# Performance work log

Hardware: AMD Instinct MI355X
Metric: run time of the kernel (lower is better)

## Reference

```python
import jax, jax.numpy as jnp
import numpy as np
from jax import lax

KSIZE = 3
STRIDE = 1
RATE = 2
FUSE_K = 3
SCALE = 10.0
DN = ('NCHW', 'OIHW', 'NCHW')


def _same_pad_amount(size, k, s):
    out = (size + s - 1) // s
    pad = max(0, (out - 1) * s + k - size)
    return pad // 2, pad - pad // 2


def extract_patches(x, k, s):
    # torch.nn.Unfold with 'same' padding; returns [B, L, C, k, k], L row-major
    B, C, H, W = x.shape
    pt, pb = _same_pad_amount(H, k, s)
    pl, pr = _same_pad_amount(W, k, s)
    xp = jnp.pad(x, ((0, 0), (0, 0), (pt, pb), (pl, pr)))
    Ho = (H + s - 1) // s
    Wo = (W + s - 1) // s
    rows = (jnp.arange(Ho) * s)[:, None] + jnp.arange(k)[None, :]  # [Ho,k]
    cols = (jnp.arange(Wo) * s)[:, None] + jnp.arange(k)[None, :]  # [Wo,k]
    p = xp[:, :, rows, :][:, :, :, :, cols]  # [B,C,Ho,k,Wo,k]
    return p.transpose(0, 2, 4, 1, 3, 5).reshape(B, Ho * Wo, C, k, k)


def setup_inputs() -> dict:
    key = jax.random.key(0)
    kf, kb = jax.random.split(key)
    f = jax.random.normal(kf, (2, 128, 128, 128), dtype=jnp.float32)
    b = jax.random.normal(kb, (2, 128, 128, 128), dtype=jnp.float32)
    mask = jnp.zeros((1, 1, 128, 128), dtype=jnp.float32)  # all patches available
    return {"f": f, "b": b, "mask": mask}


def reference(f, b, mask):
    B, C, Hr, Wr = f.shape
    kernel = 2 * RATE
    # raw background patches for final aggregation: [B, Lb, C, 4, 4]
    raw_w = extract_patches(b, kernel, RATE * STRIDE)
    # nearest downsample by rate (src_idx = i*rate)
    f_ds = f[:, :, ::RATE, ::RATE]
    b_ds = b[:, :, ::RATE, ::RATE]
    Hf, Wf = f_ds.shape[2], f_ds.shape[3]
    Hb, Wb = b_ds.shape[2], b_ds.shape[3]
    L = Hb * Wb
    # matching patches: [B, L, C, 3, 3]
    w = extract_patches(b_ds, KSIZE, STRIDE)
    # mask patches (shared across batch, torch uses m[0])
    m_ds = mask[:, :, ::RATE, ::RATE]
    m = extract_patches(m_ds, KSIZE, STRIDE)[0]  # [L,1,3,3]
    mm = (jnp.mean(m, axis=(1, 2, 3)) == 0.0).astype(f.dtype).reshape(1, L, 1, 1)
    # L2-normalize patch filters (escape_NaN added elementwise before sum, as in torch)
    wn = w / jnp.sqrt(jnp.sum(w * w + 1e-4, axis=(2, 3, 4), keepdims=True))

    def score_one(xi, wi):
        # xi [C,Hf,Wf], wi [L,C,3,3] -> [L,Hf,Wf]
        return lax.conv_general_dilated(xi[None], wi, (1, 1), [(1, 1), (1, 1)],
                                        dimension_numbers=DN)[0]

    y = jax.vmap(score_one)(f_ds, wn)  # [B, L, Hf, Wf]

    # diagonal fuse: identity 3x3 conv on the [L, Hf*Wf] score matrix, twice with transpose
    fw = jnp.eye(FUSE_K, dtype=f.dtype).reshape(1, 1, FUSE_K, FUSE_K)

    def fuse_conv(t):
        return lax.conv_general_dilated(t, fw, (1, 1), [(1, 1), (1, 1)],
                                        dimension_numbers=DN)

    y = y.reshape(B, 1, Hb * Wb, Hf * Wf)
    y = fuse_conv(y).reshape(B, Hb, Wb, Hf, Wf)
    y = y.transpose(0, 2, 1, 4, 3).reshape(B, 1, L, Hf * Wf)
    y = fuse_conv(y).reshape(B, Wb, Hb, Wf, Hf)
    y = y.transpose(0, 2, 1, 4, 3).reshape(B, L, Hf, Wf)

    y = y * mm
    y = jax.nn.softmax(y * SCALE, axis=1) * mm

    def deconv_one(a, wc):
        # conv_transpose2d(a, wc, stride=rate, padding=1); wc [L,C,4,4]
        wt = jnp.flip(wc, (-2, -1)).transpose(1, 0, 2, 3)  # [C,L,4,4]
        pad = kernel - 1 - 1
        return lax.conv_general_dilated(a[None], wt, (1, 1), [(pad, pad), (pad, pad)],
                                        lhs_dilation=(RATE, RATE),
                                        dimension_numbers=DN)[0]

    out = jax.vmap(deconv_one)(y, raw_w) / 4.0  # [B, C, Hr, Wr]
    return out
```

## Files before the change

kernel.cpp:

```cpp
#include <hip/hip_runtime.h>
#include <cstdint>

typedef _Float16 f16x8 __attribute__((ext_vector_type(8)));
typedef float f32x4 __attribute__((ext_vector_type(4)));

typedef __attribute__((address_space(1))) void gvoid;
typedef __attribute__((address_space(3))) void lvoid;

__device__ __forceinline__ void gload16(const void* g, void* l) {
    __builtin_amdgcn_global_load_lds((gvoid*)g, (lvoid*)l, 16, 0, 0);
}

__global__ __launch_bounds__(256) void downsample_kernel(const float* __restrict__ f,
                                                         const float* __restrict__ b,
                                                         float* __restrict__ fds,
                                                         float* __restrict__ bds) {
    int idx = blockIdx.x * 256 + threadIdx.x;
    const float* src = blockIdx.y ? b : f;
    float* dst = blockIdx.y ? bds : fds;
    int bb = idx >> 19;
    int r = idx & 524287;
    int c = r >> 12, a = (r >> 6) & 63, v = r & 63;
    dst[idx] = src[(size_t)bb * 2097152 + (size_t)c * 16384 + (2 * a) * 128 + 2 * v];
}

__global__ __launch_bounds__(256) void build_mm_kernel(const float* __restrict__ mask,
                                                       float* __restrict__ mm) {
    int l = blockIdx.x * 256 + threadIdx.x;
    if (l >= 4096) return;
    int i = l >> 6, j = l & 63;
    float s = 0.f;
    #pragma unroll
    for (int dy = 0; dy < 3; ++dy)
        #pragma unroll
        for (int dx = 0; dx < 3; ++dx) {
            int a = i + dy - 1, b = j + dx - 1;
            if ((unsigned)a < 64u && (unsigned)b < 64u)
                s += mask[(2 * a) * 128 + 2 * b];
        }
    mm[l] = (s == 0.0f) ? 1.0f : 0.0f;
}

__global__ __launch_bounds__(256) void build_fpatch_kernel(const float* __restrict__ fds,
                                                           _Float16* __restrict__ Fp) {
    int bb = blockIdx.x >> 12;
    int p = blockIdx.x & 4095;
    const float* fb = fds + (size_t)bb * 524288;
    _Float16* Fpb = Fp + (size_t)bb * 4718592;
    int u = p >> 6, v = p & 63;
    for (int k = threadIdx.x; k < 1152; k += 256) {
        int c = k / 9;
        int s = k - 9 * c;
        int dy = s / 3, dx = s - 3 * dy;
        int a = u + dy - 1, bcol = v + dx - 1;
        float val = 0.f;
        if ((unsigned)a < 64u && (unsigned)bcol < 64u)
            val = fb[c * 4096 + a * 64 + bcol];
        Fpb[(size_t)p * 1152 + k] = (_Float16)val;
    }
}

__global__ __launch_bounds__(256) void build_wn_kernel(const float* __restrict__ bds,
                                                       _Float16* __restrict__ Wn) {
    __shared__ float wsh[1152];
    __shared__ float red[4];
    int bb = blockIdx.x >> 12;
    int l = blockIdx.x & 4095;
    const float* bp = bds + (size_t)bb * 524288;
    _Float16* Wnb = Wn + (size_t)bb * 4718592;
    int i = l >> 6, j = l & 63;
    float sq = 0.f;
    for (int k = threadIdx.x; k < 1152; k += 256) {
        int c = k / 9;
        int s = k - 9 * c;
        int dy = s / 3, dx = s - 3 * dy;
        int a = i + dy - 1, bcol = j + dx - 1;
        float val = 0.f;
        if ((unsigned)a < 64u && (unsigned)bcol < 64u)
            val = bp[c * 4096 + a * 64 + bcol];
        wsh[k] = val;
        sq += val * val;
    }
    #pragma unroll
    for (int off = 32; off > 0; off >>= 1) sq += __shfl_xor(sq, off);
    if ((threadIdx.x & 63) == 0) red[threadIdx.x >> 6] = sq;
    __syncthreads();
    float total = red[0] + red[1] + red[2] + red[3] + 0.1152f;
    float rinv = 1.0f / sqrtf(total);
    for (int k = threadIdx.x; k < 1152; k += 256)
        Wnb[(size_t)l * 1152 + k] = (_Float16)(wsh[k] * rinv);
}

__global__ __launch_bounds__(256) void build_vt_kernel(const float* __restrict__ b,
                                                       _Float16* __restrict__ Vt) {
    int bb = blockIdx.x >> 11;
    int n = blockIdx.x & 2047;
    const float* bp = b + (size_t)bb * 2097152;
    _Float16* Vtb = Vt + (size_t)bb * 8388608;
    int c = n >> 4, r = n & 15, rh = r >> 2, rw = r & 3;
    const float* bc = bp + (size_t)c * 16384;
    for (int l = threadIdx.x; l < 4096; l += 256) {
        int lh = l >> 6, lw = l & 63;
        int row = 2 * lh + rh - 1, col = 2 * lw + rw - 1;
        float val = 0.f;
        if ((unsigned)row < 128u && (unsigned)col < 128u)
            val = bc[row * 128 + col];
        Vtb[(size_t)n * 4096 + l] = (_Float16)val;
    }
}

__global__ __launch_bounds__(256) void gemm1_kernel(const _Float16* __restrict__ Fp,
                                                    const _Float16* __restrict__ Wn,
                                                    _Float16* __restrict__ S0) {
    __shared__ __align__(16) _Float16 As[128 * 32];
    __shared__ __align__(16) _Float16 Bs[128 * 32];
    const int z = blockIdx.z;
    const _Float16* A = Fp + (size_t)z * 4718592;
    const _Float16* Bt = Wn + (size_t)z * 4718592;
    _Float16* C = S0 + (size_t)z * 16777216;
    const int tid = threadIdx.x;
    const int lane = tid & 63;
    const int wave = tid >> 6;
    const int quad = lane >> 4;
    const int l16 = lane & 15;
    const int bm = blockIdx.y * 128;
    const int bn = blockIdx.x * 128;
    const int waveM = (wave >> 1) * 64;
    const int waveN = (wave & 1) * 64;
    const int K = 1152;

    f32x4 acc[4][4] = {};

    const int rowS = tid >> 2;
    const int colS = (tid & 3) * 8;

    for (int k0 = 0; k0 < K; k0 += 32) {
        #pragma unroll
        for (int i = 0; i < 2; ++i) {
            const _Float16* g = A + (size_t)(bm + i * 64 + rowS) * K + k0 + colS;
            gload16(g, &As[i * 2048 + tid * 8]);
        }
        #pragma unroll
        for (int i = 0; i < 2; ++i) {
            const _Float16* g = Bt + (size_t)(bn + i * 64 + rowS) * K + k0 + colS;
            gload16(g, &Bs[i * 2048 + tid * 8]);
        }
        __syncthreads();
        f16x8 a_frag[4], b_frag[4];
        #pragma unroll
        for (int mi = 0; mi < 4; ++mi)
            a_frag[mi] = *(const f16x8*)&As[(waveM + mi * 16 + l16) * 32 + quad * 8];
        #pragma unroll
        for (int ni = 0; ni < 4; ++ni)
            b_frag[ni] = *(const f16x8*)&Bs[(waveN + ni * 16 + l16) * 32 + quad * 8];
        #pragma unroll
        for (int mi = 0; mi < 4; ++mi)
            #pragma unroll
            for (int ni = 0; ni < 4; ++ni)
                acc[mi][ni] = __builtin_amdgcn_mfma_f32_16x16x32_f16(
                    a_frag[mi], b_frag[ni], acc[mi][ni], 0, 0, 0);
        __syncthreads();
    }

    #pragma unroll
    for (int mi = 0; mi < 4; ++mi)
        #pragma unroll
        for (int ni = 0; ni < 4; ++ni)
            #pragma unroll
            for (int r = 0; r < 4; ++r) {
                int row = bm + waveM + mi * 16 + quad * 4 + r;
                int col = bn + waveN + ni * 16 + l16;
                C[(size_t)row * 4096 + col] = (_Float16)acc[mi][ni][r];
            }
}

__global__ __launch_bounds__(256) void gemm2_kernel(const _Float16* __restrict__ Vt,
                                                    const _Float16* __restrict__ att0,
                                                    const _Float16* __restrict__ att1,
                                                    _Float16* __restrict__ OTh) {
    __shared__ __align__(16) _Float16 As[128 * 64];
    __shared__ __align__(16) _Float16 Bs[128 * 64];
    const int z = blockIdx.z;
    const _Float16* A = Vt + (size_t)z * 8388608;
    const _Float16* Bt = z ? att1 : att0;
    _Float16* C = OTh + (size_t)z * 8388608;
    const int tid = threadIdx.x;
    const int lane = tid & 63;
    const int wave = tid >> 6;
    const int quad = lane >> 4;
    const int l16 = lane & 15;
    const int bm = blockIdx.y * 128;
    const int bn = blockIdx.x * 128;
    const int waveM = (wave >> 1) * 64;
    const int waveN = (wave & 1) * 64;
    const int K = 4096;

    f32x4 acc[4][4] = {};

    const int rowS = tid >> 3;
    const int cbs = ((tid & 7) ^ (rowS & 7)) * 8;

    for (int k0 = 0; k0 < K; k0 += 64) {
        #pragma unroll
        for (int i = 0; i < 4; ++i) {
            const _Float16* g = A + (size_t)(bm + i * 32 + rowS) * K + k0 + cbs;
            gload16(g, &As[i * 2048 + tid * 8]);
        }
        #pragma unroll
        for (int i = 0; i < 4; ++i) {
            const _Float16* g = Bt + (size_t)(bn + i * 32 + rowS) * K + k0 + cbs;
            gload16(g, &Bs[i * 2048 + tid * 8]);
        }
        __syncthreads();
        #pragma unroll
        for (int h = 0; h < 2; ++h) {
            f16x8 a_frag[4], b_frag[4];
            #pragma unroll
            for (int mi = 0; mi < 4; ++mi) {
                int r = waveM + mi * 16 + l16;
                int q = h * 4 + quad;
                a_frag[mi] = *(const f16x8*)&As[r * 64 + ((q ^ (r & 7)) * 8)];
            }
            #pragma unroll
            for (int ni = 0; ni < 4; ++ni) {
                int r = waveN + ni * 16 + l16;
                int q = h * 4 + quad;
                b_frag[ni] = *(const f16x8*)&Bs[r * 64 + ((q ^ (r & 7)) * 8)];
            }
            #pragma unroll
            for (int mi = 0; mi < 4; ++mi)
                #pragma unroll
                for (int ni = 0; ni < 4; ++ni)
                    acc[mi][ni] = __builtin_amdgcn_mfma_f32_16x16x32_f16(
                        a_frag[mi], b_frag[ni], acc[mi][ni], 0, 0, 0);
        }
        __syncthreads();
    }

    #pragma unroll
    for (int mi = 0; mi < 4; ++mi)
        #pragma unroll
        for (int ni = 0; ni < 4; ++ni)
            #pragma unroll
            for (int r = 0; r < 4; ++r) {
                int row = bm + waveM + mi * 16 + quad * 4 + r;
                int col = bn + waveN + ni * 16 + l16;
                C[(size_t)row * 4096 + col] = (_Float16)acc[mi][ni][r];
            }
}

__global__ __launch_bounds__(256) void fuse_softmax_kernel(const _Float16* __restrict__ S0,
                                                           const float* __restrict__ mm,
                                                           _Float16* __restrict__ att0,
                                                           _Float16* __restrict__ att1) {
    __shared__ float red[4];
    const int tid = threadIdx.x;
    const int lane = tid & 63;
    const int wave = tid >> 6;
    int g = blockIdx.x;
    int p_global = ((g & 7) << 10) | (g >> 3);
    const int bb = p_global >> 12;
    const int p = p_global & 4095;
    const _Float16* S = S0 + (size_t)bb * 16777216;
    _Float16* att = bb ? att1 : att0;
    const int pbase = ((p & 63) << 6) | (p >> 6);

    float acc[16];
    #pragma unroll
    for (int k = 0; k < 16; ++k) acc[k] = 0.f;

    #pragma unroll
    for (int t2 = -1; t2 <= 1; ++t2) {
        int b2 = pbase + t2;
        if ((unsigned)b2 >= 4096u) continue;
        int pp = ((b2 & 63) << 6) | (b2 >> 6);
        #pragma unroll
        for (int t1 = -1; t1 <= 1; ++t1) {
            int rr = pp + t1;
            if ((unsigned)rr >= 4096u) continue;
            const _Float16* row = S + (size_t)rr * 4096;
            #pragma unroll
            for (int k = 0; k < 16; ++k) {
                int l = k * 256 + tid;
                int i = (k * 256 + wave * 64) >> 6;
                int it2 = i + t2;
                if (it2 >= 0 && it2 < 64) {
                    int c = l + t2 * 64 + t1;
                    if ((unsigned)c < 4096u)
                        acc[k] += (float)row[c];
                } else if (it2 == 64) {
                    if (lane <= 62) {
                        int c = lane + 1 + t1;
                        if ((unsigned)c < 4096u) acc[k] += (float)row[c];
                    }
                } else {
                    if (lane >= 1) {
                        int c = 4031 + lane + t1;
                        if ((unsigned)c < 4096u) acc[k] += (float)row[c];
                    }
                }
            }
        }
    }

    float mv[16];
    float lmax = -1e30f;
    #pragma unroll
    for (int k = 0; k < 16; ++k) {
        int l = k * 256 + tid;
        mv[k] = mm[l];
        float lg = acc[k] * mv[k] * 10.0f;
        acc[k] = lg;
        lmax = fmaxf(lmax, lg);
    }
    #pragma unroll
    for (int off = 32; off > 0; off >>= 1) lmax = fmaxf(lmax, __shfl_xor(lmax, off));
    if (lane == 0) red[wave] = lmax;
    __syncthreads();
    lmax = fmaxf(fmaxf(red[0], red[1]), fmaxf(red[2], red[3]));
    __syncthreads();

    float lsum = 0.f;
    #pragma unroll
    for (int k = 0; k < 16; ++k) {
        float e = __expf(acc[k] - lmax);
        acc[k] = e;
        lsum += e;
    }
    #pragma unroll
    for (int off = 32; off > 0; off >>= 1) lsum += __shfl_xor(lsum, off);
    if (lane == 0) red[wave] = lsum;
    __syncthreads();
    float inv = 1.0f / (red[0] + red[1] + red[2] + red[3]);
    #pragma unroll
    for (int k = 0; k < 16; ++k) {
        int l = k * 256 + tid;
        att[(size_t)p * 4096 + l] = (_Float16)(acc[k] * inv * mv[k]);
    }
}

__global__ __launch_bounds__(256) void assemble_kernel(const _Float16* __restrict__ OTh,
                                                       float* __restrict__ out) {
    int idx = blockIdx.x * 256 + threadIdx.x;
    int bb = idx >> 21;
    int w = idx & 2097151;
    const _Float16* OTb = OTh + (size_t)bb * 8388608;
    int x = w & 127, y = (w >> 7) & 127, c = w >> 14;
    int r0 = (y + 1) & 1, s0 = (x + 1) & 1;
    float acc = 0.f;
    #pragma unroll
    for (int a = 0; a < 2; ++a) {
        int rh = r0 + 2 * a;
        int ph = (y + 1 - rh) >> 1;
        if ((unsigned)ph < 64u) {
            #pragma unroll
            for (int bq = 0; bq < 2; ++bq) {
                int rw = s0 + 2 * bq;
                int pw = (x + 1 - rw) >> 1;
                if ((unsigned)pw < 64u)
                    acc += (float)OTb[(size_t)(c * 16 + rh * 4 + rw) * 4096 + ph * 64 + pw];
            }
        }
    }
    out[idx] = 0.25f * acc;
}

extern "C" void kernel_launch(void* const* d_in, const int* in_sizes, int n_in,
                              void* d_out, int out_size, void* d_ws, size_t ws_size,
                              hipStream_t stream) {
    const float* f = (const float*)d_in[0];
    const float* b = (const float*)d_in[1];
    const float* mask = (const float*)d_in[2];
    float* out = (float*)d_out;
    char* ws = (char*)d_ws;

    float* mm = (float*)ws;
    _Float16* Fp = (_Float16*)(ws + 16384);
    _Float16* Wn = (_Float16*)(ws + 16384 + 18874368);
    _Float16* att0 = (_Float16*)(ws + 16384);
    _Float16* S0 = (_Float16*)(ws + 37765120);
    _Float16* Vt = (_Float16*)(ws + 37765120);
    _Float16* OTh = (_Float16*)(ws + 37765120 + 33554432);
    float* fds = (float*)(ws + 104873984);
    float* bds = (float*)(ws + 104873984 + 4194304);
    _Float16* att1 = (_Float16*)(ws + 104873984);

    downsample_kernel<<<dim3(4096, 2), 256, 0, stream>>>(f, b, fds, bds);
    build_mm_kernel<<<16, 256, 0, stream>>>(mask, mm);
    build_fpatch_kernel<<<8192, 256, 0, stream>>>(fds, Fp);
    build_wn_kernel<<<8192, 256, 0, stream>>>(bds, Wn);

    gemm1_kernel<<<dim3(32, 32, 2), 256, 0, stream>>>(Fp, Wn, S0);
    fuse_softmax_kernel<<<8192, 256, 0, stream>>>(S0, mm, att0, att1);

    build_vt_kernel<<<4096, 256, 0, stream>>>(b, Vt);
    gemm2_kernel<<<dim3(32, 16, 2), 256, 0, stream>>>(Vt, att0, att1, OTh);
    assemble_kernel<<<16384, 256, 0, stream>>>(OTh, out);
}
```

Measured before the change: 464.9 us.

## Rewrite gemm2 with 256x256 tiles, 8 waves and double-buffered LDS pipeline

The second GEMM (Vt x attention) moves from 128x128 tiles with 4 waves and a single LDS buffer to 256x256 tiles with 8 waves. It adds double-buffered async global-to-LDS loads interleaved with MFMA phases, using explicit vmcnt waits, raw barriers, s_setprio around MFMA bursts and a new LDS swizzle. The aim is to hide global load latency and raise arithmetic intensity per tile. The risks are higher register pressure from the 32 accumulators and fewer blocks (256 total) relative to the CU count.

```diff
diff --git a/kernel.cpp b/kernel.cpp
--- a/kernel.cpp
+++ b/kernel.cpp
@@ -10,6 +10,13 @@
 __device__ __forceinline__ void gload16(const void* g, void* l) {
     __builtin_amdgcn_global_load_lds((gvoid*)g, (lvoid*)l, 16, 0, 0);
 }
+
+__device__ __forceinline__ void bar() {
+    asm volatile("" ::: "memory");
+    __builtin_amdgcn_s_barrier();
+    asm volatile("" ::: "memory");
+}
+#define WAITV(N) asm volatile("s_waitcnt vmcnt(" #N ")" ::: "memory")
 
 __global__ __launch_bounds__(256) void downsample_kernel(const float* __restrict__ f,
                                                          const float* __restrict__ b,
@@ -174,12 +181,12 @@
             }
 }
 
-__global__ __launch_bounds__(256) void gemm2_kernel(const _Float16* __restrict__ Vt,
-                                                    const _Float16* __restrict__ att0,
-                                                    const _Float16* __restrict__ att1,
-                                                    _Float16* __restrict__ OTh) {
-    __shared__ __align__(16) _Float16 As[128 * 64];
-    __shared__ __align__(16) _Float16 Bs[128 * 64];
+__global__ __launch_bounds__(512, 2) void gemm2_kernel(const _Float16* __restrict__ Vt,
+                                                       const _Float16* __restrict__ att0,
+                                                       const _Float16* __restrict__ att1,
+                                                       _Float16* __restrict__ OTh) {
+    __shared__ __align__(16) _Float16 As[2][2][8192];
+    __shared__ __align__(16) _Float16 Bs[2][2][8192];
     const int z = blockIdx.z;
     const _Float16* A = Vt + (size_t)z * 8388608;
     const _Float16* Bt = z ? att1 : att0;
@@ -189,62 +196,109 @@
     const int wave = tid >> 6;
     const int quad = lane >> 4;
     const int l16 = lane & 15;
-    const int bm = blockIdx.y * 128;
-    const int bn = blockIdx.x * 128;
-    const int waveM = (wave >> 1) * 64;
-    const int waveN = (wave & 1) * 64;
-    const int K = 4096;
-
-    f32x4 acc[4][4] = {};
-
-    const int rowS = tid >> 3;
-    const int cbs = ((tid & 7) ^ (rowS & 7)) * 8;
-
-    for (int k0 = 0; k0 < K; k0 += 64) {
-        #pragma unroll
-        for (int i = 0; i < 4; ++i) {
-            const _Float16* g = A + (size_t)(bm + i * 32 + rowS) * K + k0 + cbs;
-            gload16(g, &As[i * 2048 + tid * 8]);
-        }
-        #pragma unroll
-        for (int i = 0; i < 4; ++i) {
-            const _Float16* g = Bt + (size_t)(bn + i * 32 + rowS) * K + k0 + cbs;
-            gload16(g, &Bs[i * 2048 + tid * 8]);
-        }
-        __syncthreads();
-        #pragma unroll
-        for (int h = 0; h < 2; ++h) {
-            f16x8 a_frag[4], b_frag[4];
-            #pragma unroll
-            for (int mi = 0; mi < 4; ++mi) {
-                int r = waveM + mi * 16 + l16;
-                int q = h * 4 + quad;
-                a_frag[mi] = *(const f16x8*)&As[r * 64 + ((q ^ (r & 7)) * 8)];
-            }
-            #pragma unroll
-            for (int ni = 0; ni < 4; ++ni) {
-                int r = waveN + ni * 16 + l16;
-                int q = h * 4 + quad;
-                b_frag[ni] = *(const f16x8*)&Bs[r * 64 + ((q ^ (r & 7)) * 8)];
-            }
-            #pragma unroll
-            for (int mi = 0; mi < 4; ++mi)
-                #pragma unroll
-                for (int ni = 0; ni < 4; ++ni)
-                    acc[mi][ni] = __builtin_amdgcn_mfma_f32_16x16x32_f16(
-                        a_frag[mi], b_frag[ni], acc[mi][ni], 0, 0, 0);
-        }
-        __syncthreads();
-    }
-
-    #pragma unroll
-    for (int mi = 0; mi < 4; ++mi)
+    const int wm = wave >> 2;
+    const int wn = wave & 3;
+    const int bm = blockIdx.y * 256;
+    const int bn = blockIdx.x * 256;
+
+    f32x4 acc[8][4] = {};
+    f16x8 afr[4], bfr[4];
+
+    const int s0 = tid, s1 = 512 + tid;
+    const int sr0 = s0 >> 2, sr1 = s1 >> 2;
+    const int r0 = sr0 ^ ((sr0 >> 2) & 1);
+    const int r1 = sr1 ^ ((sr1 >> 2) & 1);
+    const int q0 = (s0 & 3) ^ (r0 & 3);
+    const int q1 = (s1 & 3) ^ (r1 & 3);
+    const int offA0 = (bm + r0) * 4096 + q0 * 8;
+    const int offA1 = (bm + r1) * 4096 + q1 * 8;
+    const int offB0 = (bn + r0) * 4096 + q0 * 8;
+    const int offB1 = (bn + r1) * 4096 + q1 * 8;
+
+#define STAGE_A(buf, kt, kh) do {                                          \
+        gload16(A + offA0 + (kt) * 64 + (kh) * 32, &As[buf][kh][tid * 8]); \
+        gload16(A + offA1 + (kt) * 64 + (kh) * 32, &As[buf][kh][4096 + tid * 8]); \
+    } while (0)
+#define STAGE_B(buf, kt, kh) do {                                          \
+        gload16(Bt + offB0 + (kt) * 64 + (kh) * 32, &Bs[buf][kh][tid * 8]); \
+        gload16(Bt + offB1 + (kt) * 64 + (kh) * 32, &Bs[buf][kh][4096 + tid * 8]); \
+    } while (0)
+
+    const int c2 = (l16 >> 2) & 1;
+    const int rdoff = ((l16 ^ c2) * 32) + ((quad ^ (l16 & 3)) * 8);
+
+    auto LDA = [&](int buf, int kh, int mh) {
+        #pragma unroll
+        for (int mi = 0; mi < 4; ++mi)
+            afr[mi] = *(const f16x8*)&As[buf][kh][(wm * 128 + (mh * 4 + mi) * 16) * 32 + rdoff];
+    };
+    auto LDB = [&](int buf, int kh) {
         #pragma unroll
         for (int ni = 0; ni < 4; ++ni)
+            bfr[ni] = *(const f16x8*)&Bs[buf][kh][(wn * 64 + ni * 16) * 32 + rdoff];
+    };
+    auto MM = [&](int mh) {
+        __builtin_amdgcn_s_setprio(1);
+        #pragma unroll
+        for (int mi = 0; mi < 4; ++mi)
+            #pragma unroll
+            for (int ni = 0; ni < 4; ++ni)
+                acc[mh * 4 + mi][ni] = __builtin_amdgcn_mfma_f32_16x16x32_f16(
+                    afr[mi], bfr[ni], acc[mh * 4 + mi][ni], 0, 0, 0);
+        __builtin_amdgcn_s_setprio(0);
+    };
+
+    STAGE_A(0, 0, 0); STAGE_B(0, 0, 0);
+    STAGE_A(0, 0, 1); STAGE_B(0, 0, 1);
+    STAGE_A(1, 1, 0); STAGE_B(1, 1, 0);
+    WAITV(4);
+    bar();
+
+    #pragma unroll 1
+    for (int i = 0; i < 31; ++i) {
+        const int t0 = 2 * i;
+        LDA(0, 0, 0); LDB(0, 0); STAGE_A(1, t0 + 1, 1);
+        bar(); MM(0); bar();
+        LDA(0, 0, 1); STAGE_B(1, t0 + 1, 1);
+        bar(); MM(1); bar();
+        LDA(0, 1, 0); LDB(0, 1); STAGE_A(0, t0 + 2, 0);
+        bar(); MM(0); bar();
+        LDA(0, 1, 1); STAGE_B(0, t0 + 2, 0);
+        bar(); MM(1); WAITV(4); bar();
+        LDA(1, 0, 0); LDB(1, 0); STAGE_A(0, t0 + 2, 1);
+        bar(); MM(0); bar();
+        LDA(1, 0, 1); STAGE_B(0, t0 + 2, 1);
+        bar(); MM(1); bar();
+        LDA(1, 1, 0); LDB(1, 1); STAGE_A(1, t0 + 3, 0);
+        bar(); MM(0); bar();
+        LDA(1, 1, 1); STAGE_B(1, t0 + 3, 0);
+        bar(); MM(1); WAITV(4); bar();
+    }
+
+    LDA(0, 0, 0); LDB(0, 0); STAGE_A(1, 63, 1);
+    bar(); MM(0); bar();
+    LDA(0, 0, 1); STAGE_B(1, 63, 1);
+    bar(); MM(1); bar();
+    LDA(0, 1, 0); LDB(0, 1);
+    bar(); MM(0); bar();
+    LDA(0, 1, 1);
+    bar(); MM(1); WAITV(0); bar();
+    LDA(1, 0, 0); LDB(1, 0); bar(); MM(0); bar();
+    LDA(1, 0, 1);            bar(); MM(1); bar();
+    LDA(1, 1, 0); LDB(1, 1); bar(); MM(0); bar();
+    LDA(1, 1, 1);            bar(); MM(1); bar();
+
+#undef STAGE_A
+#undef STAGE_B
+
+    #pragma unroll
+    for (int mi = 0; mi < 8; ++mi)
+        #pragma unroll
+        for (int ni = 0; ni < 4; ++ni)
             #pragma unroll
             for (int r = 0; r < 4; ++r) {
-                int row = bm + waveM + mi * 16 + quad * 4 + r;
-                int col = bn + waveN + ni * 16 + l16;
+                int row = bm + wm * 128 + mi * 16 + quad * 4 + r;
+                int col = bn + wn * 64 + ni * 16 + l16;
                 C[(size_t)row * 4096 + col] = (_Float16)acc[mi][ni][r];
             }
 }
@@ -394,6 +448,6 @@
     fuse_softmax_kernel<<<8192, 256, 0, stream>>>(S0, mm, att0, att1);
 
     build_vt_kernel<<<4096, 256, 0, stream>>>(b, Vt);
-    gemm2_kernel<<<dim3(32, 16, 2), 256, 0, stream>>>(Vt, att0, att1, OTh);
+    gemm2_kernel<<<dim3(16, 8, 2), 512, 0, stream>>>(Vt, att0, att1, OTh);
     assemble_kernel<<<16384, 256, 0, stream>>>(OTh, out);
 }
```

Result: faster. 438.6 us (-5.7%).
